# Performance work log

Hardware: AMD Instinct MI355X
Metric: run time of the kernel (lower is better)

Reference implementation:

```python
import jax, jax.numpy as jnp
import numpy as np

B, T, D = 2, 512, 512
E, K = 8, 2
N_CONV, N_MAMBA = 4, 4
KCONV = 7            # conv-expert depthwise kernel
DI = 2 * D           # expert hidden width (expand=2), also Mamba d_inner
DS = 16              # Mamba d_state
DCONV = 4            # Mamba depthwise conv kernel
DTR = 32             # dt_rank = ceil(d_model/16)
WIN = 64             # entropy sliding window


def dw_causal_conv(h, w, b):
    # h: (B,T,C), w: (C,k), b: (C,). Depthwise causal conv (left pad k-1).
    k = w.shape[-1]
    hp = jnp.pad(h, ((0, 0), (k - 1, 0), (0, 0))).transpose(0, 2, 1)  # (B,C,T+k-1)
    out = jax.lax.conv_general_dilated(
        hp, w[:, None, :], (1,), 'VALID',
        dimension_numbers=('NCH', 'OIH', 'NCH'), feature_group_count=h.shape[-1])
    return out.transpose(0, 2, 1) + b


def spectral_entropy(x):
    v = x.mean(-1)                                   # (B,T)
    c1 = jnp.cumsum(v, axis=1)
    c2 = jnp.cumsum(v * v, axis=1)
    sh = lambda c: jnp.pad(c, ((0, 0), (WIN, 0)))[:, :c.shape[1]]
    mu = (c1 - sh(c1)) / WIN
    mu2 = (c2 - sh(c2)) / WIN
    var = jax.nn.relu(mu2 - mu * mu)
    return ((jnp.log(var + 1e-6) + 10.0) / 20.0)[..., None]   # (B,T,1)


def conv_expert(x, fi_w, fi_b, cw, cb, fo_w, fo_b):
    h = jax.nn.gelu(x @ fi_w.T + fi_b)
    h = dw_causal_conv(h, cw, cb)
    return jax.nn.gelu(h) @ fo_w.T + fo_b


def selective_scan(u, delta, A, Bm, Cm, Dm):
    # u, delta: (B,T,DI); A: (DI,DS); Bm, Cm: (B,T,DS); Dm: (DI,)
    dA = jnp.exp(delta[..., None] * A)                          # (B,T,DI,DS)
    dBu = delta[..., None] * Bm[:, :, None, :] * u[..., None]   # (B,T,DI,DS)

    def step(h, inp):
        dA_t, dBu_t, C_t = inp
        h = dA_t * h + dBu_t
        return h, jnp.einsum('bds,bs->bd', h, C_t)

    h0 = jnp.zeros((u.shape[0], A.shape[0], A.shape[1]), u.dtype)
    _, ys = jax.lax.scan(step, h0, (dA.swapaxes(0, 1), dBu.swapaxes(0, 1), Cm.swapaxes(0, 1)))
    return ys.swapaxes(0, 1) + u * Dm


def mamba_expert(x, in_w, cw, cb, xp_w, dt_w, dt_b, Alog, Dm, out_w):
    u, z = jnp.split(x @ in_w.T, 2, axis=-1)            # (B,T,DI) each
    u = jax.nn.silu(dw_causal_conv(u, cw, cb))
    proj = u @ xp_w.T                                    # (B,T,DTR+2*DS)
    dt, Bm, Cm = proj[..., :DTR], proj[..., DTR:DTR + DS], proj[..., DTR + DS:]
    delta = jax.nn.softplus(dt @ dt_w.T + dt_b)
    y = selective_scan(u, delta, -jnp.exp(Alog), Bm, Cm, Dm)
    return (y * jax.nn.silu(z)) @ out_w.T


def setup_inputs() -> dict:
    key = jax.random.key(0)
    ks = iter(jax.random.split(key, 32))
    n = lambda shape, s=0.02: jax.random.normal(next(ks), shape, jnp.float32) * s
    return dict(
        x=jax.random.normal(next(ks), (B, T, D), jnp.float32),
        norm_w=jnp.ones((D,), jnp.float32),
        gate_w=n((E, D)), ent_w=n((E, 1)), ent_b=jnp.zeros((E,), jnp.float32),
        temp=jnp.ones((1,), jnp.float32),
        conv_fc_in_w=n((N_CONV, DI, D)), conv_fc_in_b=jnp.zeros((N_CONV, DI), jnp.float32),
        conv_dw_w=n((N_CONV, DI, KCONV), 0.1), conv_dw_b=jnp.zeros((N_CONV, DI), jnp.float32),
        conv_fc_out_w=n((N_CONV, D, DI)), conv_fc_out_b=jnp.zeros((N_CONV, D), jnp.float32),
        mam_in_w=n((N_MAMBA, 2 * DI, D)),
        mam_conv_w=n((N_MAMBA, DI, DCONV), 0.1), mam_conv_b=jnp.zeros((N_MAMBA, DI), jnp.float32),
        mam_xproj_w=n((N_MAMBA, DTR + 2 * DS, DI)),
        mam_dt_w=n((N_MAMBA, DI, DTR)), mam_dt_b=jnp.full((N_MAMBA, DI), -4.0, jnp.float32),
        mam_Alog=jnp.tile(jnp.log(jnp.arange(1, DS + 1, dtype=jnp.float32)), (N_MAMBA, DI, 1)),
        mam_D=jnp.ones((N_MAMBA, DI), jnp.float32),
        mam_out_w=n((N_MAMBA, D, DI)),
    )


def reference(x, norm_w, gate_w, ent_w, ent_b, temp,
              conv_fc_in_w, conv_fc_in_b, conv_dw_w, conv_dw_b, conv_fc_out_w, conv_fc_out_b,
              mam_in_w, mam_conv_w, mam_conv_b, mam_xproj_w, mam_dt_w, mam_dt_b,
              mam_Alog, mam_D, mam_out_w):
    residual = x
    xn = x * jax.lax.rsqrt(jnp.mean(x * x, -1, keepdims=True) + 1e-6) * norm_w
    ent = spectral_entropy(xn)
    logits = xn @ gate_w.T + ent @ ent_w.T + ent_b
    logits = logits / (jnp.abs(temp) + 1e-6)             # (B,T,E)
    rw, sel = jax.lax.top_k(logits, K)
    rw = jax.nn.softmax(rw, axis=-1)
    # load-balance aux loss on post-temperature logits
    counts = jax.nn.one_hot(sel, E, dtype=jnp.float32).sum(2)
    aux = E * (counts.mean((0, 1)) * jax.nn.softmax(logits, -1).mean((0, 1))).sum()
    # dense expert application, masked-combine (matches torch module)
    out = jnp.zeros_like(xn)
    for e in range(N_CONV):
        wm = jnp.where(sel == e, rw, 0.0).sum(-1)
        y = conv_expert(xn, conv_fc_in_w[e], conv_fc_in_b[e], conv_dw_w[e], conv_dw_b[e],
                        conv_fc_out_w[e], conv_fc_out_b[e])
        out = out + y * wm[..., None]
    for m in range(N_MAMBA):
        e = N_CONV + m
        wm = jnp.where(sel == e, rw, 0.0).sum(-1)
        y = mamba_expert(xn, mam_in_w[m], mam_conv_w[m], mam_conv_b[m], mam_xproj_w[m],
                         mam_dt_w[m], mam_dt_b[m], mam_Alog[m], mam_D[m], mam_out_w[m])
        out = out + y * wm[..., None]
    return out + residual, aux
```

## Files before the change

kernel.cpp:

```cpp
#include <hip/hip_runtime.h>
#include <math.h>

#define B_    2
#define T_    512
#define D_    512
#define E_    8
#define DI_   1024
#define DS_   16
#define DTR_  32
#define WIN_  64
#define BT_   (B_*T_)
#define BTD_  (BT_*D_)
#define NC_   16
#define LCH_  32

typedef unsigned short u16;
typedef __attribute__((ext_vector_type(8))) short bf16x8;
typedef __attribute__((ext_vector_type(4))) float f32x4;

__device__ __forceinline__ float gelu_f(float x) {
    float x3 = x * x * x;
    return 0.5f * x * (1.0f + tanhf(0.7978845608028654f * (x + 0.044715f * x3)));
}
__device__ __forceinline__ float silu_f(float x) {
    return x / (1.0f + __expf(-x));
}
__device__ __forceinline__ float softplus_f(float x) {
    return (x > 20.0f) ? x : log1pf(__expf(x));
}
__device__ __forceinline__ u16 f2bf(float x) {
    union { float f; unsigned u; } v; v.f = x;
    unsigned r = v.u + 0x7fffu + ((v.u >> 16) & 1u);
    return (u16)(r >> 16);
}
__device__ __forceinline__ float bf2f(u16 x) {
    union { unsigned u; float f; } v; v.u = ((unsigned)x) << 16; return v.f;
}
__device__ __forceinline__ void gload_lds16(const u16* g, u16* l) {
    __builtin_amdgcn_global_load_lds((const __attribute__((address_space(1))) void*)g,
                                     (__attribute__((address_space(3))) void*)l, 16, 0, 0);
}

#define DW7T_ 10747904
#define DW4T_ 10776576
__global__ __launch_bounds__(256) void convert_weights_kernel(
    const float4* __restrict__ cfi, const float4* __restrict__ minw,
    const float4* __restrict__ cfo, const float4* __restrict__ mow,
    const float4* __restrict__ mxp, const float* __restrict__ cdw,
    const float* __restrict__ mcw, u16* __restrict__ dst)
{
    int i = blockIdx.x * 256 + threadIdx.x;
    if (i < 2686976) {
        float4 v; size_t dg;
        if (i < 524288) {
            int e = i >> 17, r = i & 131071;
            v = cfi[i]; dg = (size_t)e * 393216 + r;
        } else if (i < 1572864) {
            int off = i - 524288;
            int e = off >> 18, r = off & 262143;
            v = minw[off]; dg = (size_t)e * 393216 + 131072 + r;
        } else if (i < 2097152) {
            v = cfo[i - 1572864]; dg = i;
        } else if (i < 2621440) {
            v = mow[i - 2097152]; dg = i;
        } else {
            v = mxp[i - 2621440]; dg = i;
        }
        ushort4 o;
        o.x = f2bf(v.x); o.y = f2bf(v.y); o.z = f2bf(v.z); o.w = f2bf(v.w);
        *(ushort4*)(dst + dg * 4) = o;
    } else if (i < 2686976 + 45056) {
        int k = i - 2686976;
        if (k < 28672) {
            int z = k / 7168, r = k % 7168;
            int c = r / 7, j = r % 7;
            dst[DW7T_ + z * 7168 + j * 1024 + c] = f2bf(cdw[k]);
        } else {
            int k2 = k - 28672;
            int z = k2 / 4096, r = k2 % 4096;
            int c = r / 4, j = r % 4;
            dst[DW4T_ + z * 4096 + j * 1024 + c] = f2bf(mcw[k2]);
        }
    }
}

__global__ __launch_bounds__(256) void rmsnorm_kernel(
    const float* __restrict__ x, const float* __restrict__ nw,
    float* __restrict__ xn, u16* __restrict__ xnb, float* __restrict__ v)
{
    int t = blockIdx.x;
    const float* xr = x + (size_t)t * D_;
    float s = 0.f;
    for (int i = threadIdx.x; i < D_; i += 256) { float a = xr[i]; s += a * a; }
    __shared__ float sb[4];
    __shared__ float sb2[4];
    for (int o = 32; o > 0; o >>= 1) s += __shfl_down(s, o);
    if ((threadIdx.x & 63) == 0) sb[threadIdx.x >> 6] = s;
    __syncthreads();
    float tot = sb[0] + sb[1] + sb[2] + sb[3];
    float scale = rsqrtf(tot / (float)D_ + 1e-6f);
    float vs = 0.f;
    for (int i = threadIdx.x; i < D_; i += 256) {
        float a = xr[i] * scale * nw[i];
        xn[(size_t)t * D_ + i] = a;
        xnb[(size_t)t * D_ + i] = f2bf(a);
        vs += a;
    }
    for (int o = 32; o > 0; o >>= 1) vs += __shfl_down(vs, o);
    if ((threadIdx.x & 63) == 0) sb2[threadIdx.x >> 6] = vs;
    __syncthreads();
    if (threadIdx.x == 0) v[t] = (sb2[0] + sb2[1] + sb2[2] + sb2[3]) / (float)D_;
}

__global__ __launch_bounds__(256) void gating_kernel(
    const float* __restrict__ xn, const float* __restrict__ v,
    const float* __restrict__ gw, const float* __restrict__ ew,
    const float* __restrict__ eb, const float* __restrict__ temp,
    float* __restrict__ wm, float* __restrict__ probs)
{
    int wave = threadIdx.x >> 6, lane = threadIdx.x & 63;
    int t = blockIdx.x * 4 + wave;
    int tloc = t & (T_ - 1);
    int base = t - tloc;
    int j = tloc - (WIN_ - 1) + lane;
    float vv = (j >= 0) ? v[base + j] : 0.f;
    float s1 = vv, s2 = vv * vv;
#pragma unroll
    for (int o = 32; o > 0; o >>= 1) { s1 += __shfl_down(s1, o); s2 += __shfl_down(s2, o); }
    const float* xr = xn + (size_t)t * D_;
    float l[E_];
#pragma unroll
    for (int e = 0; e < E_; ++e) {
        float s = 0.f;
        for (int i = lane; i < D_; i += 64) s += xr[i] * gw[e * D_ + i];
#pragma unroll
        for (int o = 32; o > 0; o >>= 1) s += __shfl_down(s, o);
        l[e] = s;
    }
    if (lane == 0) {
        float mu  = s1 / (float)WIN_;
        float mu2 = s2 / (float)WIN_;
        float var = fmaxf(mu2 - mu * mu, 0.f);
        float ev  = (logf(var + 1e-6f) + 10.f) / 20.f;
        float ts = 1.f / (fabsf(temp[0]) + 1e-6f);
#pragma unroll
        for (int e = 0; e < E_; ++e) l[e] = (l[e] + ev * ew[e] + eb[e]) * ts;
        int i1 = 0;
        for (int e = 1; e < E_; ++e) if (l[e] > l[i1]) i1 = e;
        int i2 = -1;
        for (int e = 0; e < E_; ++e) { if (e == i1) continue; if (i2 < 0 || l[e] > l[i2]) i2 = e; }
        float e2 = __expf(l[i2] - l[i1]);
        float Z = 1.f + e2;
#pragma unroll
        for (int e = 0; e < E_; ++e) wm[t * E_ + e] = 0.f;
        wm[t * E_ + i1] = 1.f / Z;
        wm[t * E_ + i2] = e2 / Z;
        float mm = l[0];
        for (int e = 1; e < E_; ++e) mm = fmaxf(mm, l[e]);
        float Zs = 0.f; float p[E_];
#pragma unroll
        for (int e = 0; e < E_; ++e) { p[e] = __expf(l[e] - mm); Zs += p[e]; }
#pragma unroll
        for (int e = 0; e < E_; ++e) probs[t * E_ + e] = p[e] / Zs;
    }
}

__global__ __launch_bounds__(256) void compact_stats_kernel(
    const float* __restrict__ wm, const float* __restrict__ probs,
    int* __restrict__ idxl, int* __restrict__ cnt, float* __restrict__ out_aux)
{
    int e = blockIdx.x;
    int tid = threadIdx.x;
    int wid = tid >> 6, lane = tid & 63;
    __shared__ int wsum[4];
    __shared__ int base;
    __shared__ float psum[4];
    if (tid == 0) base = 0;
    __syncthreads();
    float ps = 0.f;
    for (int chunk = 0; chunk < 4; ++chunk) {
        int t = chunk * 256 + tid;
        bool f = wm[t * E_ + e] > 0.f;
        ps += probs[t * E_ + e];
        unsigned long long m = __ballot(f);
        if (lane == 0) wsum[wid] = __popcll(m);
        __syncthreads();
        int off = base;
        for (int w = 0; w < wid; ++w) off += wsum[w];
        off += __popcll(m & ((1ull << lane) - 1ull));
        if (f) idxl[e * 1024 + off] = t;
        __syncthreads();
        if (tid == 0) base += wsum[0] + wsum[1] + wsum[2] + wsum[3];
        __syncthreads();
    }
#pragma unroll
    for (int o = 32; o > 0; o >>= 1) ps += __shfl_down(ps, o);
    if (lane == 0) psum[wid] = ps;
    __syncthreads();
    if (tid == 0) {
        cnt[e] = base;
        float pt = psum[0] + psum[1] + psum[2] + psum[3];
        atomicAdd(out_aux, (float)E_ * ((float)base / (float)BT_) * (pt / (float)BT_));
    }
}


__global__ __launch_bounds__(256) void fused_in_gemm_kernel(
    const u16* __restrict__ xnb, const u16* __restrict__ wfused,
    const float* __restrict__ cfi_b, u16* __restrict__ hb, u16* __restrict__ uzb)
{
    const int z = blockIdx.z;
    const int nt = blockIdx.x;
    const bool isA = nt < 16;
    const int bn = (isA ? nt : nt - 16) * 64;
    const int bm = blockIdx.y * 64;
    const u16* A = xnb;
    const u16* W = wfused + (size_t)z * 1572864 + (isA ? 0 : 524288);

    __shared__ u16 As[64 * 64];
    __shared__ u16 Bs[64 * 64];
    const int tid  = threadIdx.x;
    const int wave = tid >> 6, lane = tid & 63;
    const int quad = lane >> 4, r16 = lane & 15;
    const int wm_ = (wave >> 1) * 32, wn = (wave & 1) * 32;

    const int s0 = tid, s1 = 256 + tid;
    const int r0 = s0 >> 3, q0 = (s0 & 7) ^ (r0 & 7);
    const int r1 = s1 >> 3, q1 = (s1 & 7) ^ (r1 & 7);
    const u16* Ag0 = A + (size_t)(bm + r0) * 512 + q0 * 8;
    const u16* Ag1 = A + (size_t)(bm + r1) * 512 + q1 * 8;
    const u16* Wg0 = W + (size_t)(bn + r0) * 512 + q0 * 8;
    const u16* Wg1 = W + (size_t)(bn + r1) * 512 + q1 * 8;

    f32x4 acc[2][2];
    const f32x4 zero = {0.f, 0.f, 0.f, 0.f};
    acc[0][0] = zero; acc[0][1] = zero; acc[1][0] = zero; acc[1][1] = zero;

    for (int k0 = 0; k0 < 512; k0 += 64) {
        gload_lds16(Ag0 + k0, As + tid * 8);
        gload_lds16(Ag1 + k0, As + (256 + tid) * 8);
        gload_lds16(Wg0 + k0, Bs + tid * 8);
        gload_lds16(Wg1 + k0, Bs + (256 + tid) * 8);
        __syncthreads();
#pragma unroll
        for (int ks = 0; ks < 2; ++ks) {
            bf16x8 af[2], bfr[2];
#pragma unroll
            for (int mi = 0; mi < 2; ++mi) {
                int row = wm_ + mi * 16 + r16;
                int p = (ks * 4 + quad) ^ (row & 7);
                af[mi] = *(const bf16x8*)(As + row * 64 + p * 8);
            }
#pragma unroll
            for (int ni = 0; ni < 2; ++ni) {
                int row = wn + ni * 16 + r16;
                int p = (ks * 4 + quad) ^ (row & 7);
                bfr[ni] = *(const bf16x8*)(Bs + row * 64 + p * 8);
            }
#pragma unroll
            for (int mi = 0; mi < 2; ++mi)
#pragma unroll
                for (int ni = 0; ni < 2; ++ni)
                    acc[mi][ni] = __builtin_amdgcn_mfma_f32_16x16x32_bf16(
                        af[mi], bfr[ni], acc[mi][ni], 0, 0, 0);
        }
        __syncthreads();
    }

#pragma unroll
    for (int mi = 0; mi < 2; ++mi) {
#pragma unroll
        for (int vv = 0; vv < 4; ++vv) {
            int m = bm + wm_ + mi * 16 + quad * 4 + vv;
#pragma unroll
            for (int ni = 0; ni < 2; ++ni) {
                int n = bn + wn + ni * 16 + r16;
                float val = acc[mi][ni][vv];
                if (isA) {
                    val = gelu_f(val + cfi_b[z * DI_ + n]);
                    hb[(size_t)z * BT_ * DI_ + (size_t)m * DI_ + n] = f2bf(val);
                } else {
                    uzb[(size_t)z * BT_ * 2048 + (size_t)m * 2048 + n] = f2bf(val);
                }
            }
        }
    }
}

__global__ __launch_bounds__(256) void out_gemm_kernel(
    const u16* __restrict__ Ab, const u16* __restrict__ Wb,
    const float* __restrict__ cfo_b, float* __restrict__ out,
    const float* __restrict__ wmv, const int* __restrict__ idxl,
    const int* __restrict__ cnt)
{
    const int z = blockIdx.z;
    const int count = cnt[z];
    const int bm = blockIdx.y * 64;
    if (bm >= count) return;
    const int bn = blockIdx.x * 64;
    const u16* A = Ab + (size_t)z * BT_ * DI_;
    const u16* W = Wb + (size_t)z * 524288;
    const int* il = idxl + z * 1024;

    __shared__ u16 As[64 * 64];
    __shared__ u16 Bs[64 * 64];
    const int tid  = threadIdx.x;
    const int wave = tid >> 6, lane = tid & 63;
    const int quad = lane >> 4, r16 = lane & 15;
    const int wm_ = (wave >> 1) * 32, wn = (wave & 1) * 32;

    const int s0 = tid, s1 = 256 + tid;
    const int r0 = s0 >> 3, q0 = (s0 & 7) ^ (r0 & 7);
    const int r1 = s1 >> 3, q1 = (s1 & 7) ^ (r1 & 7);
    const int tok0 = il[min(bm + r0, count - 1)];
    const int tok1 = il[min(bm + r1, count - 1)];
    const u16* Ag0 = A + (size_t)tok0 * 1024 + q0 * 8;
    const u16* Ag1 = A + (size_t)tok1 * 1024 + q1 * 8;
    const u16* Wg0 = W + (size_t)(bn + r0) * 1024 + q0 * 8;
    const u16* Wg1 = W + (size_t)(bn + r1) * 1024 + q1 * 8;

    f32x4 acc[2][2];
    const f32x4 zero = {0.f, 0.f, 0.f, 0.f};
    acc[0][0] = zero; acc[0][1] = zero; acc[1][0] = zero; acc[1][1] = zero;

    for (int k0 = 0; k0 < 1024; k0 += 64) {
        gload_lds16(Ag0 + k0, As + tid * 8);
        gload_lds16(Ag1 + k0, As + (256 + tid) * 8);
        gload_lds16(Wg0 + k0, Bs + tid * 8);
        gload_lds16(Wg1 + k0, Bs + (256 + tid) * 8);
        __syncthreads();
#pragma unroll
        for (int ks = 0; ks < 2; ++ks) {
            bf16x8 af[2], bfr[2];
#pragma unroll
            for (int mi = 0; mi < 2; ++mi) {
                int row = wm_ + mi * 16 + r16;
                int p = (ks * 4 + quad) ^ (row & 7);
                af[mi] = *(const bf16x8*)(As + row * 64 + p * 8);
            }
#pragma unroll
            for (int ni = 0; ni < 2; ++ni) {
                int row = wn + ni * 16 + r16;
                int p = (ks * 4 + quad) ^ (row & 7);
                bfr[ni] = *(const bf16x8*)(Bs + row * 64 + p * 8);
            }
#pragma unroll
            for (int mi = 0; mi < 2; ++mi)
#pragma unroll
                for (int ni = 0; ni < 2; ++ni)
                    acc[mi][ni] = __builtin_amdgcn_mfma_f32_16x16x32_bf16(
                        af[mi], bfr[ni], acc[mi][ni], 0, 0, 0);
        }
        __syncthreads();
    }

// ... 68 lines not shown
                int p = (kss * 4 + quad) ^ (row & 7);
                af[mi] = *(const bf16x8*)(As + row * 64 + p * 8);
            }
#pragma unroll
            for (int ni = 0; ni < 2; ++ni) {
                int row = wn + ni * 16 + r16;
                int p = (kss * 4 + quad) ^ (row & 7);
                bfr[ni] = *(const bf16x8*)(Bs + row * 64 + p * 8);
            }
#pragma unroll
            for (int mi = 0; mi < 2; ++mi)
#pragma unroll
                for (int ni = 0; ni < 2; ++ni)
                    acc[mi][ni] = __builtin_amdgcn_mfma_f32_16x16x32_bf16(
                        af[mi], bfr[ni], acc[mi][ni], 0, 0, 0);
        }
        __syncthreads();
    }

#pragma unroll
    for (int mi = 0; mi < 2; ++mi) {
#pragma unroll
        for (int vv = 0; vv < 4; ++vv) {
            int m = bm + wm_ + mi * 16 + quad * 4 + vv;
#pragma unroll
            for (int ni = 0; ni < 2; ++ni) {
                int n = bn + wn + ni * 16 + r16;
                atomicAdd(&(Cp + (size_t)z * sCe)[(size_t)m * ldc + n], acc[mi][ni][vv]);
            }
        }
    }
}

__global__ __launch_bounds__(256) void dt_gemm_kernel(
    const float* __restrict__ proj, const float* __restrict__ dtw,
    const float* __restrict__ dtb, float* __restrict__ delta)
{
    const int z = blockIdx.z;
    const float* A = proj + (size_t)z * BT_ * 64;
    const float* W = dtw + (size_t)z * DI_ * DTR_;
    const float* bias = dtb + (size_t)z * DI_;
    float* C = delta + (size_t)z * BT_ * DI_;

    __shared__ float As[16][68];
    __shared__ float Ws[16][68];
    const int bm = blockIdx.y * 64, bn = blockIdx.x * 64;
    const int tid = threadIdx.x;
    const int tx = tid & 15, ty = tid >> 4;
    const int lm = tid >> 2, lk = (tid & 3) * 4;

    const float* Ap = A + (size_t)(bm + lm) * 64 + lk;
    const float* Wp = W + (size_t)(bn + lm) * DTR_ + lk;

    float acc[4][4] = {};
    for (int k0 = 0; k0 < DTR_; k0 += 16) {
        float4 av = *(const float4*)(Ap + k0);
        float4 wv = *(const float4*)(Wp + k0);
        __syncthreads();
        As[lk + 0][lm] = av.x; As[lk + 1][lm] = av.y;
        As[lk + 2][lm] = av.z; As[lk + 3][lm] = av.w;
        Ws[lk + 0][lm] = wv.x; Ws[lk + 1][lm] = wv.y;
        Ws[lk + 2][lm] = wv.z; Ws[lk + 3][lm] = wv.w;
        __syncthreads();
#pragma unroll
        for (int k = 0; k < 16; ++k) {
            float4 a = *(const float4*)&As[k][ty * 4];
            float4 w = *(const float4*)&Ws[k][tx * 4];
            acc[0][0] += a.x * w.x; acc[0][1] += a.x * w.y; acc[0][2] += a.x * w.z; acc[0][3] += a.x * w.w;
            acc[1][0] += a.y * w.x; acc[1][1] += a.y * w.y; acc[1][2] += a.y * w.z; acc[1][3] += a.y * w.w;
            acc[2][0] += a.z * w.x; acc[2][1] += a.z * w.y; acc[2][2] += a.z * w.z; acc[2][3] += a.z * w.w;
            acc[3][0] += a.w * w.x; acc[3][1] += a.w * w.y; acc[3][2] += a.w * w.z; acc[3][3] += a.w * w.w;
        }
    }
#pragma unroll
    for (int i = 0; i < 4; ++i) {
        int m = bm + ty * 4 + i;
#pragma unroll
        for (int j = 0; j < 4; ++j) {
            int n = bn + tx * 4 + j;
            C[(size_t)m * DI_ + n] = softplus_f(acc[i][j] + bias[n]);
        }
    }
}

__global__ __launch_bounds__(256) void dwconv_fused_kernel(
    const u16* __restrict__ hb, const u16* __restrict__ w7t, const float* __restrict__ cb,
    u16* __restrict__ gb,
    const u16* __restrict__ uzb, const u16* __restrict__ w4t, const float* __restrict__ mb,
    u16* __restrict__ ucb)
{
    int idx = blockIdx.x * 256 + threadIdx.x;
    if (idx < 4 * BT_ * 128) {
        int z = idx >> 17;
        int r = idx & 131071;
        int c8 = (r & 127) * 8;
        int bt = r >> 7;
        int t = bt & (T_ - 1);
        const u16* hp = hb + (size_t)z * BT_ * DI_ + (size_t)bt * DI_ + c8;
        const u16* wp = w7t + z * 7168 + c8;
        const float* bp = cb + z * DI_ + c8;
        float acc[8];
        float4 b0 = *(const float4*)bp;
        float4 b1 = *(const float4*)(bp + 4);
        acc[0] = b0.x; acc[1] = b0.y; acc[2] = b0.z; acc[3] = b0.w;
        acc[4] = b1.x; acc[5] = b1.y; acc[6] = b1.z; acc[7] = b1.w;
#pragma unroll
        for (int j = 0; j < 7; ++j) {
            int tt = t - 6 + j;
            if (tt >= 0) {
                bf16x8 hv = *(const bf16x8*)(hp + (j - 6) * DI_);
                bf16x8 wv = *(const bf16x8*)(wp + j * 1024);
#pragma unroll
                for (int k = 0; k < 8; ++k)
                    acc[k] += bf2f((u16)hv[k]) * bf2f((u16)wv[k]);
            }
        }
        u16 o[8];
#pragma unroll
        for (int k = 0; k < 8; ++k) o[k] = f2bf(gelu_f(acc[k]));
        *(bf16x8*)(gb + (size_t)z * BT_ * DI_ + (size_t)bt * DI_ + c8) = *(bf16x8*)o;
    } else {
        int i2 = idx - 4 * BT_ * 128;
        int z = i2 >> 17;
        int r = i2 & 131071;
        int c8 = (r & 127) * 8;
        int bt = r >> 7;
        int t = bt & (T_ - 1);
        const u16* up = uzb + (size_t)z * BT_ * 2048 + (size_t)bt * 2048 + c8;
        const u16* wp = w4t + z * 4096 + c8;
        const float* bp = mb + z * DI_ + c8;
        float acc[8];
        float4 b0 = *(const float4*)bp;
        float4 b1 = *(const float4*)(bp + 4);
        acc[0] = b0.x; acc[1] = b0.y; acc[2] = b0.z; acc[3] = b0.w;
        acc[4] = b1.x; acc[5] = b1.y; acc[6] = b1.z; acc[7] = b1.w;
#pragma unroll
        for (int j = 0; j < 4; ++j) {
            int tt = t - 3 + j;
            if (tt >= 0) {
                bf16x8 uv = *(const bf16x8*)(up + (j - 3) * 2048);
                bf16x8 wv = *(const bf16x8*)(wp + j * 1024);
#pragma unroll
                for (int k = 0; k < 8; ++k)
                    acc[k] += bf2f((u16)uv[k]) * bf2f((u16)wv[k]);
            }
        }
        u16 o[8];
#pragma unroll
        for (int k = 0; k < 8; ++k) o[k] = f2bf(silu_f(acc[k]));
        *(bf16x8*)(ucb + (size_t)z * BT_ * DI_ + (size_t)bt * DI_ + c8) = *(bf16x8*)o;
    }
}

__global__ __launch_bounds__(256) void scan1_kernel(
    const float* __restrict__ delta, const u16* __restrict__ uc,
    const float* __restrict__ proj, const float* __restrict__ Alog,
    float2* __restrict__ PH)
{
    int z = blockIdx.y;
    int idx = blockIdx.x * 256 + threadIdx.x;
    int sq = idx & 3;
    int d = (idx >> 2) & (DI_ - 1);
    int c = (idx >> 12) & (NC_ - 1);
    int b = idx >> 16;
    float A[4];
    *(float4*)A = *(const float4*)(Alog + (size_t)z * DI_ * DS_ + d * DS_ + sq * 4);
#pragma unroll
    for (int s = 0; s < 4; ++s) A[s] = -__expf(A[s]);
    int t0 = c * LCH_;
    const float* dp = delta + (size_t)z * BT_ * DI_ + ((size_t)b * T_ + t0) * DI_ + d;
    const u16*   up = uc    + (size_t)z * BT_ * DI_ + ((size_t)b * T_ + t0) * DI_ + d;
    const float* pp = proj  + (size_t)z * BT_ * 64 + ((size_t)b * T_ + t0) * 64 + 32 + sq * 4;
    float h[4] = {}, P[4] = {1.f, 1.f, 1.f, 1.f};
#pragma unroll 4
    for (int t = 0; t < LCH_; ++t) {
        float del = dp[(size_t)t * DI_];
        float uv  = bf2f(up[(size_t)t * DI_]);
        float du  = del * uv;
        float Bv[4];
        *(float4*)Bv = *(const float4*)(pp + t * 64);
#pragma unroll
        for (int s = 0; s < 4; ++s) {
            float dA = __expf(del * A[s]);
            h[s] = dA * h[s] + du * Bv[s];
            P[s] *= dA;
        }
    }
    float2* o = PH + (size_t)z * (B_ * NC_ * DI_ * 16)
              + (size_t)(b * NC_ + c) * (DI_ * 16) + (size_t)d * 16 + sq * 4;
    float4 o0 = {P[0], h[0], P[1], h[1]};
    float4 o1 = {P[2], h[2], P[3], h[3]};
    *(float4*)&o[0] = o0;
    *(float4*)&o[2] = o1;
}

__global__ __launch_bounds__(256) void scan_mid_kernel(
    const float2* __restrict__ PH, float* __restrict__ H)
{
    int gid = blockIdx.x * 256 + threadIdx.x;
    int z = gid >> 15;
    int r = gid & 32767;
    int b = r >> 14;
    int ds16 = r & 16383;
    float h = 0.f;
    for (int c = 0; c < NC_; ++c) {
        size_t idx = (size_t)z * (B_ * NC_ * DI_ * 16) + ((size_t)(b * NC_ + c)) * (DI_ * 16) + ds16;
        H[idx] = h;
        float2 ph = PH[idx];
        h = ph.y + ph.x * h;
    }
}

__global__ __launch_bounds__(256) void scan2_kernel(
    const float* __restrict__ delta, const u16* __restrict__ uc,
    const float* __restrict__ proj, const float* __restrict__ Alog,
    const float* __restrict__ Dm, const float* __restrict__ H,
    const u16* __restrict__ uz, u16* __restrict__ yb)
{
    int z = blockIdx.y;
    int idx = blockIdx.x * 256 + threadIdx.x;
    int sq = idx & 3;
    int d = (idx >> 2) & (DI_ - 1);
    int c = (idx >> 12) & (NC_ - 1);
    int b = idx >> 16;
    float A[4];
    *(float4*)A = *(const float4*)(Alog + (size_t)z * DI_ * DS_ + d * DS_ + sq * 4);
#pragma unroll
    for (int s = 0; s < 4; ++s) A[s] = -__expf(A[s]);
    float Dd = Dm[(size_t)z * DI_ + d];
    float h[4];
    *(float4*)h = *(const float4*)(H + (size_t)z * (B_ * NC_ * DI_ * 16)
        + (size_t)(b * NC_ + c) * (DI_ * 16) + (size_t)d * 16 + sq * 4);
    int t0 = c * LCH_;
    const float* dp = delta + (size_t)z * BT_ * DI_ + ((size_t)b * T_ + t0) * DI_ + d;
    const u16*   up = uc    + (size_t)z * BT_ * DI_ + ((size_t)b * T_ + t0) * DI_ + d;
    const float* pp = proj  + (size_t)z * BT_ * 64 + ((size_t)b * T_ + t0) * 64 + 32 + sq * 4;
    const u16*   zp = uz    + (size_t)z * BT_ * 2048 + ((size_t)b * T_ + t0) * 2048 + DI_ + d;
    u16* yp = yb + (size_t)z * BT_ * DI_ + ((size_t)b * T_ + t0) * DI_ + d;
#pragma unroll 4
    for (int t = 0; t < LCH_; ++t) {
        float del = dp[(size_t)t * DI_];
        float uv  = bf2f(up[(size_t)t * DI_]);
        float du  = del * uv;
        float Bv[4], Cv[4];
        *(float4*)Bv = *(const float4*)(pp + t * 64);
        *(float4*)Cv = *(const float4*)(pp + t * 64 + 16);
        float y = 0.f;
#pragma unroll
        for (int s = 0; s < 4; ++s) {
            float dA = __expf(del * A[s]);
            h[s] = dA * h[s] + du * Bv[s];
            y += h[s] * Cv[s];
        }
        y += __shfl_down(y, 1, 4);
        y += __shfl_down(y, 2, 4);
        if (sq == 0) {
            y += uv * Dd;
            float zval = bf2f(zp[(size_t)t * 2048]);
            yp[(size_t)t * DI_] = f2bf(y * silu_f(zval));
        }
    }
}

extern "C" void kernel_launch(void* const* d_in, const int* in_sizes, int n_in,
                              void* d_out, int out_size, void* d_ws, size_t ws_size,
                              hipStream_t stream)
{
    const float* x      = (const float*)d_in[0];
    const float* norm_w = (const float*)d_in[1];
    const float* gate_w = (const float*)d_in[2];
    const float* ent_w  = (const float*)d_in[3];
    const float* ent_b  = (const float*)d_in[4];
    const float* temp   = (const float*)d_in[5];
    const float* cfi_w  = (const float*)d_in[6];
    const float* cfi_b  = (const float*)d_in[7];
    const float* cdw_w  = (const float*)d_in[8];
    const float* cdw_b  = (const float*)d_in[9];
    const float* cfo_w  = (const float*)d_in[10];
    const float* cfo_b  = (const float*)d_in[11];
    const float* min_w  = (const float*)d_in[12];
    const float* mcw    = (const float*)d_in[13];
    const float* mcb    = (const float*)d_in[14];
    const float* mxp    = (const float*)d_in[15];
    const float* mdtw   = (const float*)d_in[16];
    const float* mdtb   = (const float*)d_in[17];
    const float* mAlog  = (const float*)d_in[18];
    const float* mD     = (const float*)d_in[19];
    const float* mow    = (const float*)d_in[20];

    float* out = (float*)d_out;

    char* wp = (char*)d_ws;
    auto alloc = [&](size_t bytes) { char* r = wp; wp += (bytes + 255) & ~(size_t)255; return r; };

    float* xn    = (float*)alloc((size_t)BTD_ * 4);
    u16*   xnb   = (u16*)  alloc((size_t)BTD_ * 2);
    float* v     = (float*)alloc(BT_ * 4);
    float* wm    = (float*)alloc(BT_ * E_ * 4);
    float* probs = (float*)alloc(BT_ * E_ * 4);
    int*   idxl  = (int*)  alloc(E_ * 1024 * 4);
    int*   cnt   = (int*)  alloc(E_ * 4);
    u16*   wpool = (u16*)  alloc((size_t)10792960 * 2);
    u16* wfused  = wpool;
    u16* wout    = wpool + 6291456;
    u16* mxp_b16 = wpool + 10485760;
    u16* dw7t    = wpool + DW7T_;
    u16* dw4t    = wpool + DW4T_;

    char* pool = alloc((size_t)81 * 1024 * 1024);
    u16*    hb   = (u16*)pool;
    u16*    gb   = (u16*)(pool + (size_t)8 * 1024 * 1024);
    u16*    yb   = (u16*)(pool + (size_t)16 * 1024 * 1024);
    u16*    uzb  = (u16*)(pool + (size_t)24 * 1024 * 1024);
    u16*    ucb  = (u16*)(pool + (size_t)40 * 1024 * 1024);
    float*  proj = (float*)(pool + (size_t)48 * 1024 * 1024);
    float*  delta= (float*)(pool + (size_t)49 * 1024 * 1024);
    float2* sPH  = (float2*)(pool + (size_t)65 * 1024 * 1024);
    float*  sH   = (float*)hb;

    hipMemcpyAsync(out, x, (size_t)BTD_ * sizeof(float), hipMemcpyDeviceToDevice, stream);
    hipMemsetAsync(out + BTD_, 0, 4, stream);

    convert_weights_kernel<<<(2686976 + 45056 + 255) / 256, 256, 0, stream>>>(
        (const float4*)cfi_w, (const float4*)min_w, (const float4*)cfo_w,
        (const float4*)mow, (const float4*)mxp, cdw_w, mcw, wpool);

    rmsnorm_kernel<<<BT_, 256, 0, stream>>>(x, norm_w, xn, xnb, v);
    gating_kernel<<<BT_ / 4, 256, 0, stream>>>(xn, v, gate_w, ent_w, ent_b, temp, wm, probs);
    compact_stats_kernel<<<E_, 256, 0, stream>>>(wm, probs, idxl, cnt, out + BTD_);

    fused_in_gemm_kernel<<<dim3(48, 16, 4), 256, 0, stream>>>(
        xnb, wfused, cfi_b, hb, uzb);

    dwconv_fused_kernel<<<2 * 4 * BT_ * 128 / 256, 256, 0, stream>>>(
        hb, dw7t, cdw_b, gb, uzb, dw4t, mcb, ucb);

    hipMemsetAsync(proj, 0, (size_t)4 * BT_ * 64 * 4, stream);
    xproj_gemm_kernel<4><<<dim3(1, BT_ / 64, 16), 256, 0, stream>>>(
        ucb, (size_t)BT_ * DI_, DI_, mxp_b16, (size_t)64 * DI_, DI_,
        proj, (size_t)BT_ * 64, 64, DI_);
    dt_gemm_kernel<<<dim3(DI_ / 64, BT_ / 64, 4), 256, 0, stream>>>(
        proj, mdtw, mdtb, delta);

    const int NSC = B_ * NC_ * DI_ * 4 / 256;
    scan1_kernel<<<dim3(NSC, 4), 256, 0, stream>>>(delta, ucb, proj, mAlog, sPH);
    scan_mid_kernel<<<4 * B_ * DI_ * 16 / 256, 256, 0, stream>>>(sPH, sH);
    scan2_kernel<<<dim3(NSC, 4), 256, 0, stream>>>(
        delta, ucb, proj, mAlog, mD, sH, uzb, yb);

    out_gemm_kernel<<<dim3(D_ / 64, BT_ / 64, 8), 256, 0, stream>>>(
        gb, wout, cfo_b, out, wm, idxl, cnt);
}
```

Before: 322.7 us.

## Merge frontend and scan stages into cooperative kernels with grid syncs

Merges weight conversion, the residual copy, the proj zeroing, rmsnorm, gating and compaction into one cooperative kernel, separated by grid.sync calls. The three scan phases are likewise merged into one cooperative kernel of 512 blocks that loops over work units. The aim is to remove launch overhead and the separate memcpy and memset calls between small dependent stages. In exchange, the fixed 512-block grid lowers parallelism for the scan and conversion work, and it relies on cooperative residency of 2 blocks per CU.

```diff
diff --git a/kernel.cpp b/kernel.cpp
--- a/kernel.cpp
+++ b/kernel.cpp
@@ -1,5 +1,8 @@
 #include <hip/hip_runtime.h>
+#include <hip/hip_cooperative_groups.h>
 #include <math.h>
+
+namespace cg = cooperative_groups;
 
 #define B_    2
 #define T_    512
@@ -43,164 +46,175 @@
 
 #define DW7T_ 10747904
 #define DW4T_ 10776576
-__global__ __launch_bounds__(256) void convert_weights_kernel(
+
+__global__ __launch_bounds__(256, 2) void frontend_kernel(
+    const float* __restrict__ x, const float* __restrict__ nw,
     const float4* __restrict__ cfi, const float4* __restrict__ minw,
-    const float4* __restrict__ cfo, const float4* __restrict__ mow,
-    const float4* __restrict__ mxp, const float* __restrict__ cdw,
-    const float* __restrict__ mcw, u16* __restrict__ dst)
-{
-    int i = blockIdx.x * 256 + threadIdx.x;
-    if (i < 2686976) {
-        float4 v; size_t dg;
-        if (i < 524288) {
-            int e = i >> 17, r = i & 131071;
-            v = cfi[i]; dg = (size_t)e * 393216 + r;
-        } else if (i < 1572864) {
-            int off = i - 524288;
-            int e = off >> 18, r = off & 262143;
-            v = minw[off]; dg = (size_t)e * 393216 + 131072 + r;
-        } else if (i < 2097152) {
-            v = cfo[i - 1572864]; dg = i;
-        } else if (i < 2621440) {
-            v = mow[i - 2097152]; dg = i;
-        } else {
-            v = mxp[i - 2621440]; dg = i;
-        }
-        ushort4 o;
-        o.x = f2bf(v.x); o.y = f2bf(v.y); o.z = f2bf(v.z); o.w = f2bf(v.w);
-        *(ushort4*)(dst + dg * 4) = o;
-    } else if (i < 2686976 + 45056) {
-        int k = i - 2686976;
-        if (k < 28672) {
-            int z = k / 7168, r = k % 7168;
-            int c = r / 7, j = r % 7;
-            dst[DW7T_ + z * 7168 + j * 1024 + c] = f2bf(cdw[k]);
-        } else {
-            int k2 = k - 28672;
-            int z = k2 / 4096, r = k2 % 4096;
-            int c = r / 4, j = r % 4;
-            dst[DW4T_ + z * 4096 + j * 1024 + c] = f2bf(mcw[k2]);
-        }
-    }
-}
-
-__global__ __launch_bounds__(256) void rmsnorm_kernel(
-    const float* __restrict__ x, const float* __restrict__ nw,
-    float* __restrict__ xn, u16* __restrict__ xnb, float* __restrict__ v)
-{
-    int t = blockIdx.x;
-    const float* xr = x + (size_t)t * D_;
-    float s = 0.f;
-    for (int i = threadIdx.x; i < D_; i += 256) { float a = xr[i]; s += a * a; }
-    __shared__ float sb[4];
-    __shared__ float sb2[4];
-    for (int o = 32; o > 0; o >>= 1) s += __shfl_down(s, o);
-    if ((threadIdx.x & 63) == 0) sb[threadIdx.x >> 6] = s;
-    __syncthreads();
-    float tot = sb[0] + sb[1] + sb[2] + sb[3];
-    float scale = rsqrtf(tot / (float)D_ + 1e-6f);
-    float vs = 0.f;
-    for (int i = threadIdx.x; i < D_; i += 256) {
-        float a = xr[i] * scale * nw[i];
-        xn[(size_t)t * D_ + i] = a;
-        xnb[(size_t)t * D_ + i] = f2bf(a);
-        vs += a;
-    }
-    for (int o = 32; o > 0; o >>= 1) vs += __shfl_down(vs, o);
-    if ((threadIdx.x & 63) == 0) sb2[threadIdx.x >> 6] = vs;
-    __syncthreads();
-    if (threadIdx.x == 0) v[t] = (sb2[0] + sb2[1] + sb2[2] + sb2[3]) / (float)D_;
-}
-
-__global__ __launch_bounds__(256) void gating_kernel(
-    const float* __restrict__ xn, const float* __restrict__ v,
+    const float4* __restrict__ cfo, const float4* __restrict__ mow4,
+    const float4* __restrict__ mxp4, const float* __restrict__ cdw,
+    const float* __restrict__ mcw, u16* __restrict__ wpool,
     const float* __restrict__ gw, const float* __restrict__ ew,
     const float* __restrict__ eb, const float* __restrict__ temp,
-    float* __restrict__ wm, float* __restrict__ probs)
+    float* __restrict__ xn, u16* __restrict__ xnb, float* __restrict__ v,
+    float* __restrict__ wm, float* __restrict__ probs,
+    int* __restrict__ idxl, int* __restrict__ cnt,
+    float* __restrict__ out, float* __restrict__ proj)
 {
-    int wave = threadIdx.x >> 6, lane = threadIdx.x & 63;
-    int t = blockIdx.x * 4 + wave;
-    int tloc = t & (T_ - 1);
-    int base = t - tloc;
-    int j = tloc - (WIN_ - 1) + lane;
-    float vv = (j >= 0) ? v[base + j] : 0.f;
-    float s1 = vv, s2 = vv * vv;
-#pragma unroll
-    for (int o = 32; o > 0; o >>= 1) { s1 += __shfl_down(s1, o); s2 += __shfl_down(s2, o); }
-    const float* xr = xn + (size_t)t * D_;
-    float l[E_];
-#pragma unroll
-    for (int e = 0; e < E_; ++e) {
+    cg::grid_group grid = cg::this_grid();
+    const int bid = blockIdx.x, tid = threadIdx.x;
+    const int gtid = bid * 256 + tid;
+
+    for (int i = gtid; i < 2686976 + 45056; i += 512 * 256) {
+        if (i < 2686976) {
+            float4 val; size_t dg;
+            if (i < 524288) {
+                int e = i >> 17, r = i & 131071;
+                val = cfi[i]; dg = (size_t)e * 393216 + r;
+            } else if (i < 1572864) {
+                int off = i - 524288;
+                int e = off >> 18, r = off & 262143;
+                val = minw[off]; dg = (size_t)e * 393216 + 131072 + r;
+            } else if (i < 2097152) {
+                val = cfo[i - 1572864]; dg = i;
+            } else if (i < 2621440) {
+                val = mow4[i - 2097152]; dg = i;
+            } else {
+                val = mxp4[i - 2621440]; dg = i;
+            }
+            ushort4 o;
+            o.x = f2bf(val.x); o.y = f2bf(val.y); o.z = f2bf(val.z); o.w = f2bf(val.w);
+            *(ushort4*)(wpool + dg * 4) = o;
+        } else {
+            int k = i - 2686976;
+            if (k < 28672) {
+                int z = k / 7168, r = k % 7168;
+                int c = r / 7, j = r % 7;
+                wpool[DW7T_ + z * 7168 + j * 1024 + c] = f2bf(cdw[k]);
+            } else {
+                int k2 = k - 28672;
+                int z = k2 / 4096, r = k2 % 4096;
+                int c = r / 4, j = r % 4;
+                wpool[DW4T_ + z * 4096 + j * 1024 + c] = f2bf(mcw[k2]);
+            }
+        }
+    }
+
+    ((float2*)out)[gtid]          = ((const float2*)x)[gtid];
+    ((float2*)out)[gtid + 131072] = ((const float2*)x)[gtid + 131072];
+    proj[gtid] = 0.f;
+    proj[gtid + 131072] = 0.f;
+    if (gtid == 0) out[BTD_] = 0.f;
+
+    __shared__ float sb[4], sb2[4];
+    for (int rep = 0; rep < 2; ++rep) {
+        int t = bid + rep * 512;
+        const float* xr = x + (size_t)t * D_;
         float s = 0.f;
-        for (int i = lane; i < D_; i += 64) s += xr[i] * gw[e * D_ + i];
-#pragma unroll
+        for (int i = tid; i < D_; i += 256) { float a = xr[i]; s += a * a; }
         for (int o = 32; o > 0; o >>= 1) s += __shfl_down(s, o);
-        l[e] = s;
-    }
-    if (lane == 0) {
-        float mu  = s1 / (float)WIN_;
-        float mu2 = s2 / (float)WIN_;
-        float var = fmaxf(mu2 - mu * mu, 0.f);
-        float ev  = (logf(var + 1e-6f) + 10.f) / 20.f;
-        float ts = 1.f / (fabsf(temp[0]) + 1e-6f);
-#pragma unroll
-        for (int e = 0; e < E_; ++e) l[e] = (l[e] + ev * ew[e] + eb[e]) * ts;
-        int i1 = 0;
-        for (int e = 1; e < E_; ++e) if (l[e] > l[i1]) i1 = e;
-        int i2 = -1;
-        for (int e = 0; e < E_; ++e) { if (e == i1) continue; if (i2 < 0 || l[e] > l[i2]) i2 = e; }
-        float e2 = __expf(l[i2] - l[i1]);
-        float Z = 1.f + e2;
-#pragma unroll
-        for (int e = 0; e < E_; ++e) wm[t * E_ + e] = 0.f;
-        wm[t * E_ + i1] = 1.f / Z;
-        wm[t * E_ + i2] = e2 / Z;
-        float mm = l[0];
-        for (int e = 1; e < E_; ++e) mm = fmaxf(mm, l[e]);
-        float Zs = 0.f; float p[E_];
-#pragma unroll
-        for (int e = 0; e < E_; ++e) { p[e] = __expf(l[e] - mm); Zs += p[e]; }
-#pragma unroll
-        for (int e = 0; e < E_; ++e) probs[t * E_ + e] = p[e] / Zs;
-    }
-}
-
-__global__ __launch_bounds__(256) void compact_stats_kernel(
-    const float* __restrict__ wm, const float* __restrict__ probs,
-    int* __restrict__ idxl, int* __restrict__ cnt, float* __restrict__ out_aux)
-{
-    int e = blockIdx.x;
-    int tid = threadIdx.x;
-    int wid = tid >> 6, lane = tid & 63;
-    __shared__ int wsum[4];
-    __shared__ int base;
-    __shared__ float psum[4];
-    if (tid == 0) base = 0;
-    __syncthreads();
-    float ps = 0.f;
-    for (int chunk = 0; chunk < 4; ++chunk) {
-        int t = chunk * 256 + tid;
-        bool f = wm[t * E_ + e] > 0.f;
-        ps += probs[t * E_ + e];
-        unsigned long long m = __ballot(f);
-        if (lane == 0) wsum[wid] = __popcll(m);
-        __syncthreads();
-        int off = base;
-        for (int w = 0; w < wid; ++w) off += wsum[w];
-        off += __popcll(m & ((1ull << lane) - 1ull));
-        if (f) idxl[e * 1024 + off] = t;
-        __syncthreads();
-        if (tid == 0) base += wsum[0] + wsum[1] + wsum[2] + wsum[3];
-        __syncthreads();
-    }
-#pragma unroll
-    for (int o = 32; o > 0; o >>= 1) ps += __shfl_down(ps, o);
-    if (lane == 0) psum[wid] = ps;
-    __syncthreads();
-    if (tid == 0) {
-        cnt[e] = base;
-        float pt = psum[0] + psum[1] + psum[2] + psum[3];
-        atomicAdd(out_aux, (float)E_ * ((float)base / (float)BT_) * (pt / (float)BT_));
+        if ((tid & 63) == 0) sb[tid >> 6] = s;
+        __syncthreads();
+        float tot = sb[0] + sb[1] + sb[2] + sb[3];
+        float scale = rsqrtf(tot / (float)D_ + 1e-6f);
+        float vs = 0.f;
+        for (int i = tid; i < D_; i += 256) {
+            float a = xr[i] * scale * nw[i];
+            xn[(size_t)t * D_ + i] = a;
+            xnb[(size_t)t * D_ + i] = f2bf(a);
+            vs += a;
+        }
+        for (int o = 32; o > 0; o >>= 1) vs += __shfl_down(vs, o);
+        if ((tid & 63) == 0) sb2[tid >> 6] = vs;
+        __syncthreads();
+        if (tid == 0) v[t] = (sb2[0] + sb2[1] + sb2[2] + sb2[3]) / (float)D_;
+        __syncthreads();
+    }
+
+    grid.sync();
+
+    if (bid < 256) {
+        int wave = tid >> 6, lane = tid & 63;
+        int t = bid * 4 + wave;
+        int tloc = t & (T_ - 1);
+        int base = t - tloc;
+        int j = tloc - (WIN_ - 1) + lane;
+        float vv = (j >= 0) ? v[base + j] : 0.f;
+        float s1 = vv, s2 = vv * vv;
+#pragma unroll
+        for (int o = 32; o > 0; o >>= 1) { s1 += __shfl_down(s1, o); s2 += __shfl_down(s2, o); }
+        const float* xr = xn + (size_t)t * D_;
+        float l[E_];
+#pragma unroll
+        for (int e = 0; e < E_; ++e) {
+            float s = 0.f;
+            for (int i = lane; i < D_; i += 64) s += xr[i] * gw[e * D_ + i];
+#pragma unroll
+            for (int o = 32; o > 0; o >>= 1) s += __shfl_down(s, o);
+            l[e] = s;
+        }
+        if (lane == 0) {
+            float mu  = s1 / (float)WIN_;
+            float mu2 = s2 / (float)WIN_;
+            float var = fmaxf(mu2 - mu * mu, 0.f);
+            float ev  = (logf(var + 1e-6f) + 10.f) / 20.f;
+            float ts = 1.f / (fabsf(temp[0]) + 1e-6f);
+#pragma unroll
+            for (int e = 0; e < E_; ++e) l[e] = (l[e] + ev * ew[e] + eb[e]) * ts;
+            int i1 = 0;
+            for (int e = 1; e < E_; ++e) if (l[e] > l[i1]) i1 = e;
+            int i2 = -1;
+            for (int e = 0; e < E_; ++e) { if (e == i1) continue; if (i2 < 0 || l[e] > l[i2]) i2 = e; }
+            float e2 = __expf(l[i2] - l[i1]);
+            float Z = 1.f + e2;
+#pragma unroll
+            for (int e = 0; e < E_; ++e) wm[t * E_ + e] = 0.f;
+            wm[t * E_ + i1] = 1.f / Z;
+            wm[t * E_ + i2] = e2 / Z;
+            float mm = l[0];
+            for (int e = 1; e < E_; ++e) mm = fmaxf(mm, l[e]);
+            float Zs = 0.f; float p[E_];
+#pragma unroll
+            for (int e = 0; e < E_; ++e) { p[e] = __expf(l[e] - mm); Zs += p[e]; }
+#pragma unroll
+            for (int e = 0; e < E_; ++e) probs[t * E_ + e] = p[e] / Zs;
+        }
+    }
+
+    grid.sync();
+
+    if (bid < E_) {
+        int e = bid;
+        int wid = tid >> 6, lane = tid & 63;
+        __shared__ int wsum[4];
+        __shared__ int cbase;
+        __shared__ float psum[4];
+        if (tid == 0) cbase = 0;
+        __syncthreads();
+        float ps = 0.f;
+        for (int chunk = 0; chunk < 4; ++chunk) {
+            int t = chunk * 256 + tid;
+            bool f = wm[t * E_ + e] > 0.f;
+            ps += probs[t * E_ + e];
+            unsigned long long m = __ballot(f);
+            if (lane == 0) wsum[wid] = __popcll(m);
+            __syncthreads();
+            int off = cbase;
+            for (int w = 0; w < wid; ++w) off += wsum[w];
+            off += __popcll(m & ((1ull << lane) - 1ull));
+            if (f) idxl[e * 1024 + off] = t;
+            __syncthreads();
+            if (tid == 0) cbase += wsum[0] + wsum[1] + wsum[2] + wsum[3];
+            __syncthreads();
+        }
+#pragma unroll
+        for (int o = 32; o > 0; o >>= 1) ps += __shfl_down(ps, o);
+        if (lane == 0) psum[wid] = ps;
+        __syncthreads();
+        if (tid == 0) {
+            cnt[e] = cbase;
+            float pt = psum[0] + psum[1] + psum[2] + psum[3];
+            atomicAdd(&out[BTD_], (float)E_ * ((float)cbase / (float)BT_) * (pt / (float)BT_));
+        }
     }
 }
 
@@ -575,112 +589,116 @@
     }
 }
 
-__global__ __launch_bounds__(256) void scan1_kernel(
+__global__ __launch_bounds__(256, 2) void scan_coop_kernel(
     const float* __restrict__ delta, const u16* __restrict__ uc,
     const float* __restrict__ proj, const float* __restrict__ Alog,
-    float2* __restrict__ PH)
+    const float* __restrict__ Dm, const u16* __restrict__ uz,
+    float2* __restrict__ PH, float* __restrict__ H, u16* __restrict__ yb)
 {
-    int z = blockIdx.y;
-    int idx = blockIdx.x * 256 + threadIdx.x;
-    int sq = idx & 3;
-    int d = (idx >> 2) & (DI_ - 1);
-    int c = (idx >> 12) & (NC_ - 1);
-    int b = idx >> 16;
-    float A[4];
-    *(float4*)A = *(const float4*)(Alog + (size_t)z * DI_ * DS_ + d * DS_ + sq * 4);
-#pragma unroll
-    for (int s = 0; s < 4; ++s) A[s] = -__expf(A[s]);
-    int t0 = c * LCH_;
-    const float* dp = delta + (size_t)z * BT_ * DI_ + ((size_t)b * T_ + t0) * DI_ + d;
-    const u16*   up = uc    + (size_t)z * BT_ * DI_ + ((size_t)b * T_ + t0) * DI_ + d;
-    const float* pp = proj  + (size_t)z * BT_ * 64 + ((size_t)b * T_ + t0) * 64 + 32 + sq * 4;
-    float h[4] = {}, P[4] = {1.f, 1.f, 1.f, 1.f};
+    cg::grid_group grid = cg::this_grid();
+
+    for (int rep = 0; rep < 4; ++rep) {
+        int unit = blockIdx.x + rep * 512;
+        int z = unit >> 9;
+        int idx = (unit & 511) * 256 + threadIdx.x;
+        int sq = idx & 3;
+        int d = (idx >> 2) & (DI_ - 1);
+        int c = (idx >> 12) & (NC_ - 1);
+        int b = idx >> 16;
+        float A[4];
+        *(float4*)A = *(const float4*)(Alog + (size_t)z * DI_ * DS_ + d * DS_ + sq * 4);
+#pragma unroll
+        for (int s = 0; s < 4; ++s) A[s] = -__expf(A[s]);
+        int t0 = c * LCH_;
+        const float* dp = delta + (size_t)z * BT_ * DI_ + ((size_t)b * T_ + t0) * DI_ + d;
+        const u16*   up = uc    + (size_t)z * BT_ * DI_ + ((size_t)b * T_ + t0) * DI_ + d;
+        const float* pp = proj  + (size_t)z * BT_ * 64 + ((size_t)b * T_ + t0) * 64 + 32 + sq * 4;
+        float h[4] = {}, P[4] = {1.f, 1.f, 1.f, 1.f};
 #pragma unroll 4
-    for (int t = 0; t < LCH_; ++t) {
-        float del = dp[(size_t)t * DI_];
-        float uv  = bf2f(up[(size_t)t * DI_]);
-        float du  = del * uv;
-        float Bv[4];
-        *(float4*)Bv = *(const float4*)(pp + t * 64);
-#pragma unroll
-        for (int s = 0; s < 4; ++s) {
-            float dA = __expf(del * A[s]);
-            h[s] = dA * h[s] + du * Bv[s];
-            P[s] *= dA;
-        }
-    }
-    float2* o = PH + (size_t)z * (B_ * NC_ * DI_ * 16)
-              + (size_t)(b * NC_ + c) * (DI_ * 16) + (size_t)d * 16 + sq * 4;
-    float4 o0 = {P[0], h[0], P[1], h[1]};
-    float4 o1 = {P[2], h[2], P[3], h[3]};
-    *(float4*)&o[0] = o0;
-    *(float4*)&o[2] = o1;
-}
-
-__global__ __launch_bounds__(256) void scan_mid_kernel(
-    const float2* __restrict__ PH, float* __restrict__ H)
-{
-    int gid = blockIdx.x * 256 + threadIdx.x;
-    int z = gid >> 15;
-    int r = gid & 32767;
-    int b = r >> 14;
-    int ds16 = r & 16383;
-    float h = 0.f;
-    for (int c = 0; c < NC_; ++c) {
-        size_t idx = (size_t)z * (B_ * NC_ * DI_ * 16) + ((size_t)(b * NC_ + c)) * (DI_ * 16) + ds16;
-        H[idx] = h;
-        float2 ph = PH[idx];
-        h = ph.y + ph.x * h;
-    }
-}
-
-__global__ __launch_bounds__(256) void scan2_kernel(
-    const float* __restrict__ delta, const u16* __restrict__ uc,
-    const float* __restrict__ proj, const float* __restrict__ Alog,
-    const float* __restrict__ Dm, const float* __restrict__ H,
-    const u16* __restrict__ uz, u16* __restrict__ yb)
-{
-    int z = blockIdx.y;
-    int idx = blockIdx.x * 256 + threadIdx.x;
-    int sq = idx & 3;
-    int d = (idx >> 2) & (DI_ - 1);
-    int c = (idx >> 12) & (NC_ - 1);
-    int b = idx >> 16;
-    float A[4];
-    *(float4*)A = *(const float4*)(Alog + (size_t)z * DI_ * DS_ + d * DS_ + sq * 4);
-#pragma unroll
-    for (int s = 0; s < 4; ++s) A[s] = -__expf(A[s]);
-    float Dd = Dm[(size_t)z * DI_ + d];
-    float h[4];
-    *(float4*)h = *(const float4*)(H + (size_t)z * (B_ * NC_ * DI_ * 16)
-        + (size_t)(b * NC_ + c) * (DI_ * 16) + (size_t)d * 16 + sq * 4);
-    int t0 = c * LCH_;
-    const float* dp = delta + (size_t)z * BT_ * DI_ + ((size_t)b * T_ + t0) * DI_ + d;
-    const u16*   up = uc    + (size_t)z * BT_ * DI_ + ((size_t)b * T_ + t0) * DI_ + d;
-    const float* pp = proj  + (size_t)z * BT_ * 64 + ((size_t)b * T_ + t0) * 64 + 32 + sq * 4;
-    const u16*   zp = uz    + (size_t)z * BT_ * 2048 + ((size_t)b * T_ + t0) * 2048 + DI_ + d;
-    u16* yp = yb + (size_t)z * BT_ * DI_ + ((size_t)b * T_ + t0) * DI_ + d;
+        for (int t = 0; t < LCH_; ++t) {
+            float del = dp[(size_t)t * DI_];
+            float uv  = bf2f(up[(size_t)t * DI_]);
+            float du  = del * uv;
+            float Bv[4];
+            *(float4*)Bv = *(const float4*)(pp + t * 64);
+#pragma unroll
+            for (int s = 0; s < 4; ++s) {
+                float dA = __expf(del * A[s]);
+                h[s] = dA * h[s] + du * Bv[s];
+                P[s] *= dA;
+            }
+        }
+        float2* o = PH + (size_t)z * (B_ * NC_ * DI_ * 16)
+                  + (size_t)(b * NC_ + c) * (DI_ * 16) + (size_t)d * 16 + sq * 4;
+        float4 o0 = {P[0], h[0], P[1], h[1]};
+        float4 o1 = {P[2], h[2], P[3], h[3]};
+        *(float4*)&o[0] = o0;
+        *(float4*)&o[2] = o1;
+    }
+
+    grid.sync();
+
+    {
+        int gid = blockIdx.x * 256 + threadIdx.x;
+        int z = gid >> 15;
+        int r = gid & 32767;
+        int b = r >> 14;
+        int ds16 = r & 16383;
+        float h = 0.f;
+        for (int c = 0; c < NC_; ++c) {
+            size_t idx = (size_t)z * (B_ * NC_ * DI_ * 16) + ((size_t)(b * NC_ + c)) * (DI_ * 16) + ds16;
+            H[idx] = h;
+            float2 ph = PH[idx];
+            h = ph.y + ph.x * h;
+        }
+    }
+
+    grid.sync();
+
+    for (int rep = 0; rep < 4; ++rep) {
+        int unit = blockIdx.x + rep * 512;
+        int z = unit >> 9;
+        int idx = (unit & 511) * 256 + threadIdx.x;
+        int sq = idx & 3;
+        int d = (idx >> 2) & (DI_ - 1);
+        int c = (idx >> 12) & (NC_ - 1);
+        int b = idx >> 16;
+        float A[4];
+        *(float4*)A = *(const float4*)(Alog + (size_t)z * DI_ * DS_ + d * DS_ + sq * 4);
+#pragma unroll
+        for (int s = 0; s < 4; ++s) A[s] = -__expf(A[s]);
+        float Dd = Dm[(size_t)z * DI_ + d];
+        float h[4];
+        *(float4*)h = *(const float4*)(H + (size_t)z * (B_ * NC_ * DI_ * 16)
+            + (size_t)(b * NC_ + c) * (DI_ * 16) + (size_t)d * 16 + sq * 4);
+        int t0 = c * LCH_;
+        const float* dp = delta + (size_t)z * BT_ * DI_ + ((size_t)b * T_ + t0) * DI_ + d;
+        const u16*   up = uc    + (size_t)z * BT_ * DI_ + ((size_t)b * T_ + t0) * DI_ + d;
+        const float* pp = proj  + (size_t)z * BT_ * 64 + ((size_t)b * T_ + t0) * 64 + 32 + sq * 4;
+        const u16*   zp = uz    + (size_t)z * BT_ * 2048 + ((size_t)b * T_ + t0) * 2048 + DI_ + d;
+        u16* yp = yb + (size_t)z * BT_ * DI_ + ((size_t)b * T_ + t0) * DI_ + d;
 #pragma unroll 4
-    for (int t = 0; t < LCH_; ++t) {
-        float del = dp[(size_t)t * DI_];
-        float uv  = bf2f(up[(size_t)t * DI_]);
-        float du  = del * uv;
-        float Bv[4], Cv[4];
-        *(float4*)Bv = *(const float4*)(pp + t * 64);
-        *(float4*)Cv = *(const float4*)(pp + t * 64 + 16);
-        float y = 0.f;
-#pragma unroll
-        for (int s = 0; s < 4; ++s) {
-            float dA = __expf(del * A[s]);
-            h[s] = dA * h[s] + du * Bv[s];
-            y += h[s] * Cv[s];
-        }
-        y += __shfl_down(y, 1, 4);
-        y += __shfl_down(y, 2, 4);
-        if (sq == 0) {
-            y += uv * Dd;
-            float zval = bf2f(zp[(size_t)t * 2048]);
-            yp[(size_t)t * DI_] = f2bf(y * silu_f(zval));
+        for (int t = 0; t < LCH_; ++t) {
+            float del = dp[(size_t)t * DI_];
+            float uv  = bf2f(up[(size_t)t * DI_]);
+            float du  = del * uv;
+            float Bv[4], Cv[4];
+            *(float4*)Bv = *(const float4*)(pp + t * 64);
+            *(float4*)Cv = *(const float4*)(pp + t * 64 + 16);
+            float y = 0.f;
+#pragma unroll
+            for (int s = 0; s < 4; ++s) {
+                float dA = __expf(del * A[s]);
+                h[s] = dA * h[s] + du * Bv[s];
+                y += h[s] * Cv[s];
+            }
+            y += __shfl_down(y, 1, 4);
+            y += __shfl_down(y, 2, 4);
+            if (sq == 0) {
+                y += uv * Dd;
+                float zval = bf2f(zp[(size_t)t * 2048]);
+                yp[(size_t)t * DI_] = f2bf(y * silu_f(zval));
+            }
         }
     }
 }
@@ -741,16 +759,21 @@
     float2* sPH  = (float2*)(pool + (size_t)65 * 1024 * 1024);
     float*  sH   = (float*)hb;
 
-    hipMemcpyAsync(out, x, (size_t)BTD_ * sizeof(float), hipMemcpyDeviceToDevice, stream);
-    hipMemsetAsync(out + BTD_, 0, 4, stream);
-
-    convert_weights_kernel<<<(2686976 + 45056 + 255) / 256, 256, 0, stream>>>(
-        (const float4*)cfi_w, (const float4*)min_w, (const float4*)cfo_w,
-        (const float4*)mow, (const float4*)mxp, cdw_w, mcw, wpool);
-
-    rmsnorm_kernel<<<BT_, 256, 0, stream>>>(x, norm_w, xn, xnb, v);
-    gating_kernel<<<BT_ / 4, 256, 0, stream>>>(xn, v, gate_w, ent_w, ent_b, temp, wm, probs);
-    compact_stats_kernel<<<E_, 256, 0, stream>>>(wm, probs, idxl, cnt, out + BTD_);
+    {
+        const float4* cfi4 = (const float4*)cfi_w;
+        const float4* min4 = (const float4*)min_w;
+        const float4* cfo4 = (const float4*)cfo_w;
+        const float4* mow4 = (const float4*)mow;
+        const float4* mxp4 = (const float4*)mxp;
+        void* fa[] = { (void*)&x, (void*)&norm_w, (void*)&cfi4, (void*)&min4,
+                       (void*)&cfo4, (void*)&mow4, (void*)&mxp4, (void*)&cdw_w,
+                       (void*)&mcw, (void*)&wpool, (void*)&gate_w, (void*)&ent_w,
+                       (void*)&ent_b, (void*)&temp, (void*)&xn, (void*)&xnb,
+                       (void*)&v, (void*)&wm, (void*)&probs, (void*)&idxl,
+                       (void*)&cnt, (void*)&out, (void*)&proj };
+        hipLaunchCooperativeKernel((void*)frontend_kernel, dim3(512), dim3(256),
+                                   fa, 0, stream);
+    }
 
     fused_in_gemm_kernel<<<dim3(48, 16, 4), 256, 0, stream>>>(
         xnb, wfused, cfi_b, hb, uzb);
@@ -758,18 +781,18 @@
     dwconv_fused_kernel<<<2 * 4 * BT_ * 128 / 256, 256, 0, stream>>>(
         hb, dw7t, cdw_b, gb, uzb, dw4t, mcb, ucb);
 
-    hipMemsetAsync(proj, 0, (size_t)4 * BT_ * 64 * 4, stream);
     xproj_gemm_kernel<4><<<dim3(1, BT_ / 64, 16), 256, 0, stream>>>(
         ucb, (size_t)BT_ * DI_, DI_, mxp_b16, (size_t)64 * DI_, DI_,
         proj, (size_t)BT_ * 64, 64, DI_);
     dt_gemm_kernel<<<dim3(DI_ / 64, BT_ / 64, 4), 256, 0, stream>>>(
         proj, mdtw, mdtb, delta);
 
-    const int NSC = B_ * NC_ * DI_ * 4 / 256;
-    scan1_kernel<<<dim3(NSC, 4), 256, 0, stream>>>(delta, ucb, proj, mAlog, sPH);
-    scan_mid_kernel<<<4 * B_ * DI_ * 16 / 256, 256, 0, stream>>>(sPH, sH);
-    scan2_kernel<<<dim3(NSC, 4), 256, 0, stream>>>(
-        delta, ucb, proj, mAlog, mD, sH, uzb, yb);
+    {
+        void* sa[] = { (void*)&delta, (void*)&ucb, (void*)&proj, (void*)&mAlog,
+                       (void*)&mD, (void*)&uzb, (void*)&sPH, (void*)&sH, (void*)&yb };
+        hipLaunchCooperativeKernel((void*)scan_coop_kernel, dim3(512), dim3(256),
+                                   sa, 0, stream);
+    }
 
     out_gemm_kernel<<<dim3(D_ / 64, BT_ / 64, 8), 256, 0, stream>>>(
         gb, wout, cfo_b, out, wm, idxl, cnt);
```

New measurement: 687.2 us. 113% more time.
